# Kernel optimization log

Measured on AMD Instinct MI355X. Metric: run time of the kernel, lower is better.

Reference implementation:

```python
import jax, jax.numpy as jnp
import numpy as np

TOTAL_WORDS = 10000
EMBED_LEN = 100
SEQ_LEN = 80
UNITS = 128
BATCH = 4096


def setup_inputs() -> dict:
    key = jax.random.key(0)
    ks = jax.random.split(key, 8)
    s = 0.05  # small init scale to keep gates unsaturated
    return {
        "tokens": jax.random.randint(ks[0], (BATCH, SEQ_LEN), 0, TOTAL_WORDS),
        "emb": jax.random.normal(ks[1], (TOTAL_WORDS, EMBED_LEN), jnp.float32) * s,
        "W1": jax.random.normal(ks[2], (EMBED_LEN, 4 * UNITS), jnp.float32) * s,
        "U1": jax.random.normal(ks[3], (UNITS, 4 * UNITS), jnp.float32) * s,
        "b1": jnp.zeros((4 * UNITS,), jnp.float32),
        "W2": jax.random.normal(ks[4], (UNITS, 4 * UNITS), jnp.float32) * s,
        "U2": jax.random.normal(ks[5], (UNITS, 4 * UNITS), jnp.float32) * s,
        "b2": jnp.zeros((4 * UNITS,), jnp.float32),
        "Wd": jax.random.normal(ks[6], (UNITS, 1), jnp.float32) * s,
        "bd": jnp.zeros((1,), jnp.float32),
    }


def _lstm(x_seq, W, U, b, return_sequences):
    # x_seq: [B, T, D]; Keras gate order: i, f, g(c), o
    B = x_seq.shape[0]
    H = U.shape[0]

    def step(carry, x_t):
        h, c = carry
        z = x_t @ W + h @ U + b  # [B, 4H]
        i, f, g, o = jnp.split(z, 4, axis=-1)
        c = jax.nn.sigmoid(f) * c + jax.nn.sigmoid(i) * jnp.tanh(g)
        h = jax.nn.sigmoid(o) * jnp.tanh(c)
        return (h, c), h

    h0 = jnp.zeros((B, H), x_seq.dtype)
    (hT, _), hs = jax.lax.scan(step, (h0, h0), jnp.swapaxes(x_seq, 0, 1))
    return jnp.swapaxes(hs, 0, 1) if return_sequences else hT


def reference(tokens, emb, W1, U1, b1, W2, U2, b2, Wd, bd):
    x = emb[tokens]                      # [B, T, E]
    h1 = _lstm(x, W1, U1, b1, True)      # [B, T, H]
    h2 = _lstm(h1, W2, U2, b2, False)    # [B, H] (last step)
    return jax.nn.sigmoid(h2 @ Wd + bd)  # [B, 1]
```

## Files before the change

### kernel.cpp

```cpp
#include <hip/hip_runtime.h>
#include <hip/hip_bf16.h>

#define T_SEQ 80
#define EMB   100
#define HU    128
#define G4    512
#define BR    16
#define THR   512
#define LOG2E 1.44269504f

typedef __attribute__((ext_vector_type(8))) short bfrag;
typedef __attribute__((ext_vector_type(4))) float f32x4;

#define OFF_EW1P 0ull
#define OFF_U1T  10240000ull
#define OFF_U2T  (OFF_U1T + 131072ull)
#define OFF_W2T  (OFF_U2T + 131072ull)

__device__ inline unsigned short f2bf(float x) {
    __hip_bfloat16 h = __float2bfloat16(x);
    unsigned short u; __builtin_memcpy(&u, &h, 2); return u;
}
__device__ inline float bf2f(unsigned short u) {
    unsigned int v = ((unsigned int)u) << 16;
    float f; __builtin_memcpy(&f, &v, 4); return f;
}
__device__ inline float sig_p(float zp) {
    return __builtin_amdgcn_rcpf(1.f + __builtin_amdgcn_exp2f(zp));
}
__device__ inline float tanh_p(float zp) {
    return 1.f - 2.f * __builtin_amdgcn_rcpf(1.f + __builtin_amdgcn_exp2f(zp));
}
__device__ inline float tanh_r(float x) {
    return 1.f - 2.f * __builtin_amdgcn_rcpf(1.f + __builtin_amdgcn_exp2f(2.f * LOG2E * x));
}
__device__ inline float sig_r(float x) {
    return __builtin_amdgcn_rcpf(1.f + __builtin_amdgcn_exp2f(-LOG2E * x));
}
__device__ inline bfrag ld_frag(const unsigned short* buf, int row, int kk, int lhi) {
    int byte = (row * 256 + kk * 64 + lhi * 16) ^ ((row & 7) << 4);
    return *(const bfrag*)((const char*)buf + byte);
}
__device__ inline void st_h(unsigned short* buf, int rr, int u, unsigned short v) {
    int byte = ((rr * 256 + u * 2) ^ ((rr & 7) << 4));
    *(unsigned short*)((char*)buf + byte) = v;
}

#define K2_TOKS 25
#define VOCAB_BLKS 400
__global__ __launch_bounds__(512) void prep_all(
    const float* __restrict__ emb, const float* __restrict__ W1, const float* __restrict__ b1,
    const float* __restrict__ U1, const float* __restrict__ U2, const float* __restrict__ W2,
    unsigned short* __restrict__ EW1p, unsigned short* __restrict__ U1T,
    unsigned short* __restrict__ U2T, unsigned short* __restrict__ W2T) {
    const int tid = threadIdx.x;
    if (blockIdx.x < VOCAB_BLKS) {
        __shared__ float embs[K2_TOKS * EMB];
        const int tok0 = blockIdx.x * K2_TOKS;
        for (int i = tid; i < K2_TOKS * EMB; i += 512) embs[i] = emb[tok0 * EMB + i];
        __syncthreads();
        const int c = tid;
        const int g = c >> 7, u = c & 127;
        const float scale = (g == 2) ? 2.f * LOG2E : -LOG2E;
        float s[K2_TOKS];
        const float bias = b1[c];
#pragma unroll
        for (int tt = 0; tt < K2_TOKS; tt++) s[tt] = bias;
        for (int e = 0; e < EMB; e++) {
            float wv = W1[e * G4 + c];
#pragma unroll
            for (int tt = 0; tt < K2_TOKS; tt++) s[tt] += embs[tt * EMB + e] * wv;
        }
#pragma unroll
        for (int tt = 0; tt < K2_TOKS; tt++)
            EW1p[(size_t)(tok0 + tt) * G4 + u * 4 + g] = f2bf(s[tt] * scale);
    } else {
#pragma unroll
        for (int r = 0; r < 2; r++) {
            int idx = (blockIdx.x - VOCAB_BLKS) * 1024 + r * 512 + tid;
            int n = idx >> 7, k = idx & 127;
            const float scale = ((n >> 7) == 2) ? 2.f * LOG2E : -LOG2E;
            U1T[n * 128 + k] = f2bf(U1[k * 512 + n] * scale);
            U2T[n * 128 + k] = f2bf(U2[k * 512 + n] * scale);
            W2T[n * 128 + k] = f2bf(W2[k * 512 + n] * scale);
        }
    }
}

__global__ __launch_bounds__(THR, 2) void lstm_fused(
    const int* __restrict__ tokens, const unsigned short* __restrict__ EW1p,
    const unsigned short* __restrict__ U1T, const unsigned short* __restrict__ U2T,
    const unsigned short* __restrict__ W2T, const float* __restrict__ b2,
    const float* __restrict__ Wd, const float* __restrict__ bd, float* __restrict__ out) {

    __shared__ unsigned short w2lds[G4 * HU];
    __shared__ unsigned short h1b[2][BR * HU];
    __shared__ unsigned short h2b[2][BR * HU];
    __shared__ int toklds[BR * T_SEQ];

    const int tid = threadIdx.x;
    const int w   = tid >> 6;
    const int l   = tid & 63;
    const int llo = l & 15, lhi = l >> 4;
    const int u   = w * 16 + llo;
    const int r0  = blockIdx.x * BR;

    {
        for (int i = tid; i < G4 * HU / 8; i += THR) {
            int n = i >> 4, c16 = i & 15;
            int byte = (n * 256 + c16 * 16) ^ ((n & 7) << 4);
            *(uint4*)((char*)w2lds + byte) = *(const uint4*)(W2T + n * 128 + c16 * 8);
        }
    }
    for (int i = tid; i < BR * T_SEQ; i += THR) toklds[i] = tokens[r0 * T_SEQ + i];
    for (int i = tid; i < BR * HU; i += THR) { h2b[0][i] = 0; h2b[1][i] = 0; }

    bfrag u1r[4][4], u2r[4][4];
#pragma unroll
    for (int g = 0; g < 4; g++)
#pragma unroll
        for (int kk = 0; kk < 4; kk++) {
            size_t off = (size_t)(g * 128 + u) * 128 + kk * 32 + lhi * 8;
            u1r[g][kk] = *(const bfrag*)(U1T + off);
            u2r[g][kk] = *(const bfrag*)(U2T + off);
        }
    float bb[4];
#pragma unroll
    for (int g = 0; g < 4; g++) bb[g] = b2[g * 128 + u] * ((g == 2) ? 2.f * LOG2E : -LOG2E);

    float c1[4] = {0, 0, 0, 0}, c2[4] = {0, 0, 0, 0};
    ushort4 zv[4];

    __syncthreads();

#pragma unroll
    for (int j = 0; j < 4; j++) {
        int tok = toklds[(lhi * 4 + j) * T_SEQ + 0];
        zv[j] = *(const ushort4*)(EW1p + (size_t)tok * G4 + u * 4);
    }
#pragma unroll
    for (int j = 0; j < 4; j++) {
        float si = sig_p(bf2f(zv[j].x)), sf = sig_p(bf2f(zv[j].y));
        float tg = tanh_p(bf2f(zv[j].z)), so = sig_p(bf2f(zv[j].w));
        float cn = sf * c1[j] + si * tg;
        c1[j] = cn;
        st_h(h1b[0], lhi * 4 + j, u, f2bf(so * tanh_r(cn)));
    }
#pragma unroll
    for (int j = 0; j < 4; j++) {
        int tok = toklds[(lhi * 4 + j) * T_SEQ + 1];
        zv[j] = *(const ushort4*)(EW1p + (size_t)tok * G4 + u * 4);
    }
    __syncthreads();

    auto phase = [&](int sn, const unsigned short* h1p, const unsigned short* h2p,
                     unsigned short* h1n, unsigned short* h2n) {
        f32x4 acc1[4];
#pragma unroll
        for (int j = 0; j < 4; j++) {
            acc1[0][j] = bf2f(zv[j].x); acc1[1][j] = bf2f(zv[j].y);
            acc1[2][j] = bf2f(zv[j].z); acc1[3][j] = bf2f(zv[j].w);
        }
        bfrag a1[4];
#pragma unroll
        for (int kk = 0; kk < 4; kk++) a1[kk] = ld_frag(h1p, llo, kk, lhi);
#pragma unroll
        for (int j = 0; j < 4; j++) {
            int tok = toklds[(lhi * 4 + j) * T_SEQ + sn];
            zv[j] = *(const ushort4*)(EW1p + (size_t)tok * G4 + u * 4);
        }
#pragma unroll
        for (int g = 0; g < 4; g++)
#pragma unroll
            for (int kk = 0; kk < 4; kk++)
                acc1[g] = __builtin_amdgcn_mfma_f32_16x16x32_bf16(a1[kk], u1r[g][kk], acc1[g], 0, 0, 0);
#pragma unroll
        for (int j = 0; j < 4; j++) {
            float si = sig_p(acc1[0][j]), sf = sig_p(acc1[1][j]);
            float tg = tanh_p(acc1[2][j]), so = sig_p(acc1[3][j]);
            float cn = sf * c1[j] + si * tg;
            c1[j] = cn;
            st_h(h1n, lhi * 4 + j, u, f2bf(so * tanh_r(cn)));
        }
        f32x4 acc2[4];
#pragma unroll
        for (int g = 0; g < 4; g++) acc2[g] = (f32x4){bb[g], bb[g], bb[g], bb[g]};
#pragma unroll
        for (int g = 0; g < 4; g++)
#pragma unroll
            for (int kk = 0; kk < 4; kk++) {
                bfrag wf = ld_frag(w2lds, g * 128 + u, kk, lhi);
                acc2[g] = __builtin_amdgcn_mfma_f32_16x16x32_bf16(a1[kk], wf, acc2[g], 0, 0, 0);
            }
#pragma unroll
        for (int kk = 0; kk < 4; kk++) {
            bfrag a2 = ld_frag(h2p, llo, kk, lhi);
#pragma unroll
            for (int g = 0; g < 4; g++)
                acc2[g] = __builtin_amdgcn_mfma_f32_16x16x32_bf16(a2, u2r[g][kk], acc2[g], 0, 0, 0);
        }
#pragma unroll
        for (int j = 0; j < 4; j++) {
            float si = sig_p(acc2[0][j]), sf = sig_p(acc2[1][j]);
            float tg = tanh_p(acc2[2][j]), so = sig_p(acc2[3][j]);
            float cn = sf * c2[j] + si * tg;
            c2[j] = cn;
            st_h(h2n, lhi * 4 + j, u, f2bf(so * tanh_r(cn)));
        }
        __syncthreads();
    };

    phase(2, h1b[0], h2b[1], h1b[1], h2b[0]);
#pragma unroll 1
    for (int s = 2; s < T_SEQ - 1; s += 2) {
        phase(s + 1, h1b[1], h2b[0], h1b[0], h2b[1]);
        phase((s + 2 < T_SEQ) ? s + 2 : T_SEQ - 1,
              h1b[0], h2b[1], h1b[1], h2b[0]);
    }

    {
        f32x4 acc2[4];
#pragma unroll
        for (int g = 0; g < 4; g++) acc2[g] = (f32x4){bb[g], bb[g], bb[g], bb[g]};
#pragma unroll
        for (int kk = 0; kk < 4; kk++) {
            bfrag a1 = ld_frag(h1b[1], llo, kk, lhi);
#pragma unroll
            for (int g = 0; g < 4; g++) {
                bfrag wf = ld_frag(w2lds, g * 128 + u, kk, lhi);
                acc2[g] = __builtin_amdgcn_mfma_f32_16x16x32_bf16(a1, wf, acc2[g], 0, 0, 0);
            }
        }
#pragma unroll
        for (int kk = 0; kk < 4; kk++) {
            bfrag a2 = ld_frag(h2b[0], llo, kk, lhi);
#pragma unroll
            for (int g = 0; g < 4; g++)
                acc2[g] = __builtin_amdgcn_mfma_f32_16x16x32_bf16(a2, u2r[g][kk], acc2[g], 0, 0, 0);
        }
#pragma unroll
        for (int j = 0; j < 4; j++) {
            float si = sig_p(acc2[0][j]), sf = sig_p(acc2[1][j]);
            float tg = tanh_p(acc2[2][j]), so = sig_p(acc2[3][j]);
            float cn = sf * c2[j] + si * tg;
            c2[j] = cn;
            st_h(h2b[1], lhi * 4 + j, u, f2bf(so * tanh_r(cn)));
        }
    }
    __syncthreads();

    if (w == 0) {
        int r = l >> 2, q = l & 3;
        float s = 0.f;
        for (int k = q * 32; k < q * 32 + 32; k++) {
            int byte = (r * 256 + k * 2) ^ ((r & 7) << 4);
            s += bf2f(*(const unsigned short*)((const char*)h2b[1] + byte)) * Wd[k];
        }
        s += __shfl_xor(s, 1, 64);
        s += __shfl_xor(s, 2, 64);
        if (q == 0) out[r0 + r] = sig_r(s + bd[0]);
    }
}

extern "C" void kernel_launch(void* const* d_in, const int* in_sizes, int n_in,
                              void* d_out, int out_size, void* d_ws, size_t ws_size,
                              hipStream_t stream) {
    const int*   tokens = (const int*)  d_in[0];
    const float* emb    = (const float*)d_in[1];
    const float* W1     = (const float*)d_in[2];
    const float* U1     = (const float*)d_in[3];
    const float* b1     = (const float*)d_in[4];
    const float* W2     = (const float*)d_in[5];
    const float* U2     = (const float*)d_in[6];
    const float* b2     = (const float*)d_in[7];
    const float* Wd     = (const float*)d_in[8];
    const float* bd     = (const float*)d_in[9];
    float* out = (float*)d_out;

    char* ws = (char*)d_ws;
    unsigned short* EW1p = (unsigned short*)(ws + OFF_EW1P);
    unsigned short* U1T  = (unsigned short*)(ws + OFF_U1T);
    unsigned short* U2T  = (unsigned short*)(ws + OFF_U2T);
    unsigned short* W2T  = (unsigned short*)(ws + OFF_W2T);

    prep_all<<<VOCAB_BLKS + 64, 512, 0, stream>>>(emb, W1, b1, U1, U2, W2, EW1p, U1T, U2T, W2T);
    lstm_fused<<<256, THR, 0, stream>>>(tokens, EW1p, U1T, U2T, W2T, b2, Wd, bd, out);
}
```

Baseline: 286.3 us.

## Reorder LSTM step to overlap layer-2 recurrent MFMAs and prefetch W2 fragments

Within each timestep phase, both h1 and h2 fragments are loaded up front, and the layer-2 recurrent (U2) MFMAs are issued before the layer-1 gate nonlinearities so matrix work overlaps the transcendental math. W2 fragments are double-buffered from LDS one gate ahead of their use. The __syncthreads is replaced by an inline-asm lgkmcnt wait plus s_barrier, which may skip waiting on outstanding global (vmcnt) loads. The prep kernel is also split into more blocks with fewer tokens each. The cost is higher register pressure from the extra live fragments.

Result: faster. 267.3 us (-6.6%).

```diff
diff --git a/kernel.cpp b/kernel.cpp
--- a/kernel.cpp
+++ b/kernel.cpp
@@ -45,9 +45,12 @@
     int byte = ((rr * 256 + u * 2) ^ ((rr & 7) << 4));
     *(unsigned short*)((char*)buf + byte) = v;
 }
-
-#define K2_TOKS 25
-#define VOCAB_BLKS 400
+__device__ inline void barrier_lgkm() {
+    asm volatile("s_waitcnt lgkmcnt(0)\n\ts_barrier" ::: "memory");
+}
+
+#define K2_TOKS 8
+#define VOCAB_BLKS 1250
 __global__ __launch_bounds__(512) void prep_all(
     const float* __restrict__ emb, const float* __restrict__ W1, const float* __restrict__ b1,
     const float* __restrict__ U1, const float* __restrict__ U2, const float* __restrict__ W2,
@@ -155,15 +158,17 @@
 
     auto phase = [&](int sn, const unsigned short* h1p, const unsigned short* h2p,
                      unsigned short* h1n, unsigned short* h2n) {
+        bfrag a1[4], a2[4];
+#pragma unroll
+        for (int kk = 0; kk < 4; kk++) a1[kk] = ld_frag(h1p, llo, kk, lhi);
+#pragma unroll
+        for (int kk = 0; kk < 4; kk++) a2[kk] = ld_frag(h2p, llo, kk, lhi);
         f32x4 acc1[4];
 #pragma unroll
         for (int j = 0; j < 4; j++) {
             acc1[0][j] = bf2f(zv[j].x); acc1[1][j] = bf2f(zv[j].y);
             acc1[2][j] = bf2f(zv[j].z); acc1[3][j] = bf2f(zv[j].w);
         }
-        bfrag a1[4];
-#pragma unroll
-        for (int kk = 0; kk < 4; kk++) a1[kk] = ld_frag(h1p, llo, kk, lhi);
 #pragma unroll
         for (int j = 0; j < 4; j++) {
             int tok = toklds[(lhi * 4 + j) * T_SEQ + sn];
@@ -174,6 +179,17 @@
 #pragma unroll
             for (int kk = 0; kk < 4; kk++)
                 acc1[g] = __builtin_amdgcn_mfma_f32_16x16x32_bf16(a1[kk], u1r[g][kk], acc1[g], 0, 0, 0);
+        f32x4 acc2[4];
+#pragma unroll
+        for (int g = 0; g < 4; g++) acc2[g] = (f32x4){bb[g], bb[g], bb[g], bb[g]};
+#pragma unroll
+        for (int kk = 0; kk < 4; kk++)
+#pragma unroll
+            for (int g = 0; g < 4; g++)
+                acc2[g] = __builtin_amdgcn_mfma_f32_16x16x32_bf16(a2[kk], u2r[g][kk], acc2[g], 0, 0, 0);
+        bfrag wfc[4];
+#pragma unroll
+        for (int kk = 0; kk < 4; kk++) wfc[kk] = ld_frag(w2lds, 0 * 128 + u, kk, lhi);
 #pragma unroll
         for (int j = 0; j < 4; j++) {
             float si = sig_p(acc1[0][j]), sf = sig_p(acc1[1][j]);
@@ -182,22 +198,20 @@
             c1[j] = cn;
             st_h(h1n, lhi * 4 + j, u, f2bf(so * tanh_r(cn)));
         }
-        f32x4 acc2[4];
-#pragma unroll
-        for (int g = 0; g < 4; g++) acc2[g] = (f32x4){bb[g], bb[g], bb[g], bb[g]};
-#pragma unroll
-        for (int g = 0; g < 4; g++)
-#pragma unroll
-            for (int kk = 0; kk < 4; kk++) {
-                bfrag wf = ld_frag(w2lds, g * 128 + u, kk, lhi);
-                acc2[g] = __builtin_amdgcn_mfma_f32_16x16x32_bf16(a1[kk], wf, acc2[g], 0, 0, 0);
+#pragma unroll
+        for (int g = 0; g < 4; g++) {
+            bfrag wfn[4];
+            if (g < 3) {
+#pragma unroll
+                for (int kk = 0; kk < 4; kk++) wfn[kk] = ld_frag(w2lds, (g + 1) * 128 + u, kk, lhi);
             }
 #pragma unroll
-        for (int kk = 0; kk < 4; kk++) {
-            bfrag a2 = ld_frag(h2p, llo, kk, lhi);
-#pragma unroll
-            for (int g = 0; g < 4; g++)
-                acc2[g] = __builtin_amdgcn_mfma_f32_16x16x32_bf16(a2, u2r[g][kk], acc2[g], 0, 0, 0);
+            for (int kk = 0; kk < 4; kk++)
+                acc2[g] = __builtin_amdgcn_mfma_f32_16x16x32_bf16(a1[kk], wfc[kk], acc2[g], 0, 0, 0);
+            if (g < 3) {
+#pragma unroll
+                for (int kk = 0; kk < 4; kk++) wfc[kk] = wfn[kk];
+            }
         }
 #pragma unroll
         for (int j = 0; j < 4; j++) {
@@ -207,7 +221,7 @@
             c2[j] = cn;
             st_h(h2n, lhi * 4 + j, u, f2bf(so * tanh_r(cn)));
         }
-        __syncthreads();
+        barrier_lgkm();
     };
 
     phase(2, h1b[0], h2b[1], h1b[1], h2b[0]);
```
